# Kernel optimization log

Hardware: AMD Instinct MI355X
Metric: run time of the kernel (lower is better)

The kernel has to match this reference:

```python
import jax, jax.numpy as jnp
import numpy as np

D_MODEL = 2048
DT_RANK = 64


def setup_inputs() -> dict:
    key = jax.random.key(0)
    ks = jax.random.split(key, 9)
    x = jax.random.normal(ks[0], (4, 2048, D_MODEL), dtype=jnp.float32)
    A = jax.random.normal(ks[1], (D_MODEL, D_MODEL), dtype=jnp.float32)
    B = jax.random.normal(ks[2], (D_MODEL, D_MODEL), dtype=jnp.float32)
    C = jax.random.normal(ks[3], (D_MODEL, D_MODEL), dtype=jnp.float32)
    Dp = jax.random.normal(ks[4], (1, D_MODEL), dtype=jnp.float32)
    # dt_project: Linear(d_model -> dt_rank); dt_project_out: Linear(dt_rank -> d_model)
    lim1 = 1.0 / np.sqrt(D_MODEL)
    W1 = jax.random.uniform(ks[5], (DT_RANK, D_MODEL), minval=-lim1, maxval=lim1, dtype=jnp.float32)
    b1 = jax.random.uniform(ks[6], (DT_RANK,), minval=-lim1, maxval=lim1, dtype=jnp.float32)
    lim2 = 1.0 / np.sqrt(DT_RANK)
    W2 = jax.random.uniform(ks[7], (D_MODEL, DT_RANK), minval=-lim2, maxval=lim2, dtype=jnp.float32)
    b2 = jax.random.uniform(ks[8], (D_MODEL,), minval=-lim2, maxval=lim2, dtype=jnp.float32)
    return {"x": x, "A": A, "B": B, "C": C, "Dp": Dp, "W1": W1, "b1": b1, "W2": W2, "b2": b2}


def reference(x, A, B, C, Dp, W1, b1, W2, b2):
    # dt = Linear_out(gelu(Linear_in(x)))  -- torch uses exact (erf) gelu
    h = jax.nn.gelu(jnp.einsum('bld,rd->blr', x, W1) + b1, approximate=False)
    dt = jnp.einsum('blr,dr->bld', h, W2) + b2
    # per-timestep loop collapses to one batched GEMM: x @ (A+B+C)
    out = jnp.einsum('bld,ds->bls', x, A + B + C)
    return out * dt + Dp  # Dp broadcasts (1, d_model)
```

## Files before the change

kernel.cpp:

```cpp
#include <hip/hip_runtime.h>
#include <stdint.h>

#define D 2048
#define R 64
#define M_TOTAL 8192

typedef float f32x4 __attribute__((ext_vector_type(4)));
typedef __bf16 bf16x8 __attribute__((ext_vector_type(8)));
typedef unsigned short u16x8 __attribute__((ext_vector_type(8)));
typedef unsigned short u16x4 __attribute__((ext_vector_type(4)));

__device__ __forceinline__ unsigned short f2bf(float f) {
  unsigned u = __builtin_bit_cast(unsigned, f);
  u += 0x7FFFu + ((u >> 16) & 1u);
  return (unsigned short)(u >> 16);
}

__device__ __forceinline__ void gload_lds16(const void* g, void* l) {
  __builtin_amdgcn_global_load_lds(
      (const __attribute__((address_space(1))) void*)g,
      (__attribute__((address_space(3))) void*)l, 16, 0, 0);
}

__global__ void prep_kernel(const float* __restrict__ x, const float* __restrict__ A,
                            const float* __restrict__ B, const float* __restrict__ C,
                            const float* __restrict__ w1, const float* __restrict__ w2,
                            unsigned short* __restrict__ xbf, unsigned short* __restrict__ st,
                            unsigned short* __restrict__ w1bf, unsigned short* __restrict__ w2bf) {
  __shared__ unsigned short lds[64][68];
  int t = threadIdx.x;
  if (blockIdx.x < 1024) {
    int tk = blockIdx.x >> 5, tn = blockIdx.x & 31;
    int k0 = tk * 64, n0 = tn * 64;
#pragma unroll
    for (int q = 0; q < 4; ++q) {
      int row = q * 16 + (t >> 4);
      int col = (t & 15) * 4;
      size_t off = (size_t)(k0 + row) * D + n0 + col;
      float4 a = *(const float4*)(A + off);
      float4 b = *(const float4*)(B + off);
      float4 c = *(const float4*)(C + off);
      u16x4 o = { f2bf(a.x + b.x + c.x), f2bf(a.y + b.y + c.y),
                  f2bf(a.z + b.z + c.z), f2bf(a.w + b.w + c.w) };
      *(u16x4*)(&lds[row][col]) = o;
    }
    __syncthreads();
    int n = t >> 2, kc = (t & 3) * 16;
    u16x8 v0, v1;
#pragma unroll
    for (int jj = 0; jj < 8; ++jj) v0[jj] = lds[kc + jj][n];
#pragma unroll
    for (int jj = 0; jj < 8; ++jj) v1[jj] = lds[kc + 8 + jj][n];
    size_t ooff = (size_t)(n0 + n) * D + k0 + kc;
    *(u16x8*)(st + ooff) = v0;
    *(u16x8*)(st + ooff + 8) = v1;
  } else {
    const int NX4 = (M_TOTAL * D) / 4;
    const int NW4 = (R * D) / 4;
    int stride = 1024 * 256;
    for (int i = (blockIdx.x - 1024) * 256 + t; i < NX4 + 2 * NW4; i += stride) {
      const float4* src; unsigned short* dst; int j;
      if (i < NX4)            { src = (const float4*)x;  dst = xbf;  j = i; }
      else if (i < NX4 + NW4) { src = (const float4*)w1; dst = w1bf; j = i - NX4; }
      else                    { src = (const float4*)w2; dst = w2bf; j = i - NX4 - NW4; }
      float4 v = src[j];
      u16x4 o = { f2bf(v.x), f2bf(v.y), f2bf(v.z), f2bf(v.w) };
      *(u16x4*)(dst + (size_t)j * 4) = o;
    }
  }
}

__global__ __launch_bounds__(256) void h_kernel(const unsigned short* __restrict__ xbf,
                                                const unsigned short* __restrict__ w1bf,
                                                const float* __restrict__ b1,
                                                unsigned short* __restrict__ hbf) {
  __shared__ unsigned short sX[4 * 2048];
  __shared__ unsigned short sW[4 * 2048];
  int t = threadIdx.x;
  int w = t >> 6, l = t & 63;
  int lm = l & 15, lk = l >> 4;
  int m0 = blockIdx.x * 64;
  f32x4 acc[4] = {};

  const unsigned short* srcX = xbf + (size_t)(m0 + (t & 63)) * D + (t >> 6) * 8;
  const unsigned short* srcW = w1bf + (size_t)(t & 63) * D + (t >> 6) * 8;
  const int dstw = w * 512;

#define HSTAGE(kt) do { \
    gload_lds16(srcX + (kt) * 32, sX + ((kt) & 3) * 2048 + dstw); \
    gload_lds16(srcW + (kt) * 32, sW + ((kt) & 3) * 2048 + dstw); } while (0)

  HSTAGE(0); HSTAGE(1); HSTAGE(2);
  asm volatile("s_waitcnt vmcnt(4)" ::: "memory");
  __builtin_amdgcn_s_barrier();

#pragma unroll 1
  for (int kt = 0; kt < 64; ++kt) {
    const unsigned short* bX = sX + (kt & 3) * 2048;
    const unsigned short* bW = sW + (kt & 3) * 2048;
    bf16x8 a = __builtin_bit_cast(bf16x8, *(const u16x8*)(bX + lk * 512 + (w * 16 + lm) * 8));
    bf16x8 bw[4];
#pragma unroll
    for (int j = 0; j < 4; ++j)
      bw[j] = __builtin_bit_cast(bf16x8, *(const u16x8*)(bW + lk * 512 + (j * 16 + lm) * 8));
    if (kt + 3 < 64) HSTAGE(kt + 3);
#pragma unroll
    for (int j = 0; j < 4; ++j)
      acc[j] = __builtin_amdgcn_mfma_f32_16x16x32_bf16(a, bw[j], acc[j], 0, 0, 0);
    if (kt < 61) asm volatile("s_waitcnt vmcnt(4)" ::: "memory");
    else         asm volatile("s_waitcnt vmcnt(0)" ::: "memory");
    __builtin_amdgcn_s_barrier();
  }
#undef HSTAGE

  int m_base = m0 + w * 16 + lk * 4;
#pragma unroll
  for (int j = 0; j < 4; ++j) {
    int n = j * 16 + lm;
    float bv = b1[n];
#pragma unroll
    for (int r = 0; r < 4; ++r) {
      float v = acc[j][r] + bv;
      float g = 0.5f * v * (1.0f + erff(v * 0.70710678118654752f));
      hbf[(size_t)(m_base + r) * R + n] = f2bf(g);
    }
  }
}

__global__ __launch_bounds__(512, 2) void gemm_kernel(
    const unsigned short* __restrict__ xbf, const unsigned short* __restrict__ st,
    const unsigned short* __restrict__ hbf, const unsigned short* __restrict__ w2bf,
    const float* __restrict__ b2, const float* __restrict__ dp,
    float* __restrict__ out) {
  __shared__ unsigned short sA[2 * 16384];
  __shared__ unsigned short sB[2 * 16384];
  const int tid = threadIdx.x;
  const int w = tid >> 6, l = tid & 63, lk = l >> 4, lm = l & 15;
  const int wm = w >> 2, wn = w & 3;
  int bid = blockIdx.x;
  int wg = (bid & 7) * 32 + (bid >> 3);
  int mb = wg >> 3, nb = wg & 7;
  int m0 = mb * 256, n0 = nb * 256;

  const int kg = (tid & 7) ^ ((tid >> 3) & 7);
  const unsigned short* gA = xbf + (size_t)(m0 + (tid >> 3)) * D + kg * 8;
  const unsigned short* gB = st + (size_t)(n0 + (tid >> 3)) * D + kg * 8;
  const int dstw = w * 512;

  const int s7 = lm & 7;
  const int gsw0 = (lk ^ s7) * 8;
  const int gsw1 = ((4 | lk) ^ s7) * 8;
  const int arow = (wm * 128 + lm) * 64;
  const int brow = (wn * 64 + lm) * 64;

  f32x4 acc[8][4] = {};

#define STAGE(gptr, sbuf, T, h) do { \
    const unsigned short* g_ = (gptr) + (size_t)((h) * 128) * D + (T) * 64; \
    unsigned short* d_ = (sbuf) + (((T) & 1) * 16384 + (h) * 8192 + dstw); \
    gload_lds16(g_, d_); \
    gload_lds16(g_ + 64 * D, d_ + 4096); } while (0)

#define LD8(buf, off) __builtin_bit_cast(bf16x8, *(const u16x8*)((buf) + (off)))

  STAGE(gA, sA, 0, 0); STAGE(gA, sA, 0, 1);
  STAGE(gB, sB, 0, 0); STAGE(gB, sB, 0, 1);
  STAGE(gB, sB, 1, 0); STAGE(gB, sB, 1, 1);
  asm volatile("s_waitcnt vmcnt(4)" ::: "memory");
  __builtin_amdgcn_s_barrier();

  const int NT = D / 64;
#pragma unroll 1
  for (int kt = 0; kt < NT; ++kt) {
    const unsigned short* bufA = sA + (kt & 1) * 16384;
    const unsigned short* bufB = sB + (kt & 1) * 16384;
    bf16x8 a[4][2], b0[2][2], b1[2][2];

    #pragma unroll
    for (int i = 0; i < 4; ++i) {
      a[i][0] = LD8(bufA, arow + i * 1024 + gsw0);
      a[i][1] = LD8(bufA, arow + i * 1024 + gsw1);
    }
    #pragma unroll
    for (int j = 0; j < 2; ++j) {
      b0[j][0] = LD8(bufB, brow + j * 1024 + gsw0);
      b0[j][1] = LD8(bufB, brow + j * 1024 + gsw1);
    }
    if (kt + 1 < NT) STAGE(gA, sA, kt + 1, 0);
    __builtin_amdgcn_s_barrier();
    asm volatile("s_waitcnt lgkmcnt(0)" ::: "memory");
    __builtin_amdgcn_s_setprio(1);
    #pragma unroll
    for (int i = 0; i < 4; ++i)
      #pragma unroll
      for (int j = 0; j < 2; ++j) {
        acc[i][j] = __builtin_amdgcn_mfma_f32_16x16x32_bf16(a[i][0], b0[j][0], acc[i][j], 0, 0, 0);
        acc[i][j] = __builtin_amdgcn_mfma_f32_16x16x32_bf16(a[i][1], b0[j][1], acc[i][j], 0, 0, 0);
      }
    __builtin_amdgcn_s_setprio(0);
    __builtin_amdgcn_s_barrier();

    #pragma unroll
    for (int j = 0; j < 2; ++j) {
      b1[j][0] = LD8(bufB, brow + (j + 2) * 1024 + gsw0);
      b1[j][1] = LD8(bufB, brow + (j + 2) * 1024 + gsw1);
    }
    if (kt + 1 < NT) STAGE(gA, sA, kt + 1, 1);
    __builtin_amdgcn_s_barrier();
    asm volatile("s_waitcnt lgkmcnt(0)" ::: "memory");
    __builtin_amdgcn_s_setprio(1);
    #pragma unroll
    for (int i = 0; i < 4; ++i)
      #pragma unroll
      for (int j = 0; j < 2; ++j) {
        acc[i][j + 2] = __builtin_amdgcn_mfma_f32_16x16x32_bf16(a[i][0], b1[j][0], acc[i][j + 2], 0, 0, 0);
        acc[i][j + 2] = __builtin_amdgcn_mfma_f32_16x16x32_bf16(a[i][1], b1[j][1], acc[i][j + 2], 0, 0, 0);
      }
    __builtin_amdgcn_s_setprio(0);
    __builtin_amdgcn_s_barrier();

    #pragma unroll
    for (int i = 0; i < 4; ++i) {
      a[i][0] = LD8(bufA, arow + (i + 4) * 1024 + gsw0);
      a[i][1] = LD8(bufA, arow + (i + 4) * 1024 + gsw1);
    }
    if (kt + 2 < NT) STAGE(gB, sB, kt + 2, 0);
    __builtin_amdgcn_s_barrier();
    asm volatile("s_waitcnt lgkmcnt(0)" ::: "memory");
    __builtin_amdgcn_s_setprio(1);
    #pragma unroll
    for (int i = 0; i < 4; ++i)
      #pragma unroll
      for (int j = 0; j < 2; ++j) {
        acc[i + 4][j + 2] = __builtin_amdgcn_mfma_f32_16x16x32_bf16(a[i][0], b1[j][0], acc[i + 4][j + 2], 0, 0, 0);
        acc[i + 4][j + 2] = __builtin_amdgcn_mfma_f32_16x16x32_bf16(a[i][1], b1[j][1], acc[i + 4][j + 2], 0, 0, 0);
      }
    __builtin_amdgcn_s_setprio(0);
    __builtin_amdgcn_s_barrier();

    if (kt + 2 < NT) STAGE(gB, sB, kt + 2, 1);
    __builtin_amdgcn_s_setprio(1);
    #pragma unroll
    for (int i = 0; i < 4; ++i)
      #pragma unroll
      for (int j = 0; j < 2; ++j) {
        acc[i + 4][j] = __builtin_amdgcn_mfma_f32_16x16x32_bf16(a[i][0], b0[j][0], acc[i + 4][j], 0, 0, 0);
        acc[i + 4][j] = __builtin_amdgcn_mfma_f32_16x16x32_bf16(a[i][1], b0[j][1], acc[i + 4][j], 0, 0, 0);
      }
    __builtin_amdgcn_s_setprio(0);
    if (kt < NT - 2) asm volatile("s_waitcnt vmcnt(4)" ::: "memory");
    else             asm volatile("s_waitcnt vmcnt(0)" ::: "memory");
    __builtin_amdgcn_s_barrier();
  }

  bf16x8 wb0[4], wb1[4];
  float b2v[4], dpv[4];
#pragma unroll
  for (int j = 0; j < 4; ++j) {
    int n = n0 + wn * 64 + j * 16 + lm;
    const u16x8* wp = (const u16x8*)(w2bf + (size_t)n * R + lk * 8);
    wb0[j] = __builtin_bit_cast(bf16x8, wp[0]);
    wb1[j] = __builtin_bit_cast(bf16x8, wp[4]);
    b2v[j] = b2[n];
    dpv[j] = dp[n];
  }
#pragma unroll
  for (int mi = 0; mi < 8; ++mi) {
    int hrow = m0 + wm * 128 + mi * 16 + lm;
    const u16x8* hp = (const u16x8*)(hbf + (size_t)hrow * R + lk * 8);
    bf16x8 ha0 = __builtin_bit_cast(bf16x8, hp[0]);
    bf16x8 ha1 = __builtin_bit_cast(bf16x8, hp[4]);
    int mbase = m0 + wm * 128 + mi * 16 + lk * 4;
#pragma unroll
    for (int j = 0; j < 4; ++j) {
      f32x4 dt = {};
      dt = __builtin_amdgcn_mfma_f32_16x16x32_bf16(ha0, wb0[j], dt, 0, 0, 0);
      dt = __builtin_amdgcn_mfma_f32_16x16x32_bf16(ha1, wb1[j], dt, 0, 0, 0);
      int n = n0 + wn * 64 + j * 16 + lm;
#pragma unroll
      for (int r = 0; r < 4; ++r) {
        float val = acc[mi][j][r] * (dt[r] + b2v[j]) + dpv[j];
        out[(size_t)(mbase + r) * D + n] = val;
      }
    }
  }
#undef STAGE
#undef LD8
}

extern "C" void kernel_launch(void* const* d_in, const int* in_sizes, int n_in,
                              void* d_out, int out_size, void* d_ws, size_t ws_size,
                              hipStream_t stream) {
  const float* x  = (const float*)d_in[0];
  const float* A  = (const float*)d_in[1];
  const float* B  = (const float*)d_in[2];
  const float* C  = (const float*)d_in[3];
  const float* Dp = (const float*)d_in[4];
  const float* W1 = (const float*)d_in[5];
  const float* b1 = (const float*)d_in[6];
  const float* W2 = (const float*)d_in[7];
  const float* b2 = (const float*)d_in[8];
  float* out = (float*)d_out;

  uint8_t* ws = (uint8_t*)d_ws;
  unsigned short* xbf  = (unsigned short*)ws;
  unsigned short* st   = (unsigned short*)(ws + (32u << 20));
  unsigned short* w1bf = (unsigned short*)(ws + (40u << 20));
  unsigned short* w2bf = (unsigned short*)(ws + (40u << 20) + (256u << 10));
  unsigned short* hbf  = (unsigned short*)(ws + (41u << 20));

  prep_kernel<<<2048, 256, 0, stream>>>(x, A, B, C, W1, W2, xbf, st, w1bf, w2bf);
  h_kernel<<<128, 256, 0, stream>>>(xbf, w1bf, b1, hbf);
  gemm_kernel<<<256, 512, 0, stream>>>(xbf, st, hbf, w2bf, b2, Dp, out);
}
```

Measured before the change: 118.9 us.

## Fuse x conversion and dt-projection GEMM into prep kernel; reschedule GEMM prefetch

New measurement: 119.0 us. Within noise of the previous version (+0.1%).

```diff
diff --git a/kernel.cpp b/kernel.cpp
--- a/kernel.cpp
+++ b/kernel.cpp
@@ -22,15 +22,70 @@
       (__attribute__((address_space(3))) void*)l, 16, 0, 0);
 }
 
-__global__ void prep_kernel(const float* __restrict__ x, const float* __restrict__ A,
-                            const float* __restrict__ B, const float* __restrict__ C,
-                            const float* __restrict__ w1, const float* __restrict__ w2,
-                            unsigned short* __restrict__ xbf, unsigned short* __restrict__ st,
-                            unsigned short* __restrict__ w1bf, unsigned short* __restrict__ w2bf) {
-  __shared__ unsigned short lds[64][68];
+__global__ __launch_bounds__(256) void prep_kernel(
+    const float* __restrict__ x, const float* __restrict__ A,
+    const float* __restrict__ B, const float* __restrict__ C,
+    const float* __restrict__ w1, const float* __restrict__ b1,
+    const float* __restrict__ w2,
+    unsigned short* __restrict__ xbf, unsigned short* __restrict__ st,
+    unsigned short* __restrict__ w2bf, unsigned short* __restrict__ hbf) {
+  __shared__ unsigned short plds[10240];
   int t = threadIdx.x;
-  if (blockIdx.x < 1024) {
-    int tk = blockIdx.x >> 5, tn = blockIdx.x & 31;
+  int bx = blockIdx.x;
+  if (bx < 128) {
+    int m0 = bx * 64;
+    int row = t >> 2, c8 = (t & 3) * 8;
+    const float* xp = x + (size_t)(m0 + row) * D + c8;
+    const float* wp = w1 + (size_t)row * D + c8;
+    unsigned short* xop = xbf + (size_t)(m0 + row) * D + c8;
+    unsigned short* sX = plds;
+    unsigned short* sW = plds + 5120;
+    int w = t >> 6, lm = t & 15, lk = (t & 63) >> 4;
+    f32x4 acc[4] = {};
+    float4 rx0 = *(const float4*)(xp);
+    float4 rx1 = *(const float4*)(xp + 4);
+    float4 rw0 = *(const float4*)(wp);
+    float4 rw1 = *(const float4*)(wp + 4);
+#pragma unroll 1
+    for (int kt = 0; kt < 64; ++kt) {
+      int buf = (kt & 1) * 2560;
+      u16x8 ox = { f2bf(rx0.x), f2bf(rx0.y), f2bf(rx0.z), f2bf(rx0.w),
+                   f2bf(rx1.x), f2bf(rx1.y), f2bf(rx1.z), f2bf(rx1.w) };
+      u16x8 ow = { f2bf(rw0.x), f2bf(rw0.y), f2bf(rw0.z), f2bf(rw0.w),
+                   f2bf(rw1.x), f2bf(rw1.y), f2bf(rw1.z), f2bf(rw1.w) };
+      *(u16x8*)(sX + buf + row * 40 + c8) = ox;
+      *(u16x8*)(sW + buf + row * 40 + c8) = ow;
+      *(u16x8*)(xop + kt * 32) = ox;
+      __syncthreads();
+      if (kt < 63) {
+        rx0 = *(const float4*)(xp + (kt + 1) * 32);
+        rx1 = *(const float4*)(xp + (kt + 1) * 32 + 4);
+        rw0 = *(const float4*)(wp + (kt + 1) * 32);
+        rw1 = *(const float4*)(wp + (kt + 1) * 32 + 4);
+      }
+      bf16x8 a = __builtin_bit_cast(bf16x8, *(const u16x8*)(sX + buf + (w * 16 + lm) * 40 + lk * 8));
+#pragma unroll
+      for (int j = 0; j < 4; ++j) {
+        bf16x8 b = __builtin_bit_cast(bf16x8, *(const u16x8*)(sW + buf + (j * 16 + lm) * 40 + lk * 8));
+        acc[j] = __builtin_amdgcn_mfma_f32_16x16x32_bf16(a, b, acc[j], 0, 0, 0);
+      }
+    }
+    int m_base = m0 + w * 16 + lk * 4;
+#pragma unroll
+    for (int j = 0; j < 4; ++j) {
+      int n = j * 16 + lm;
+      float bv = b1[n];
+#pragma unroll
+      for (int r = 0; r < 4; ++r) {
+        float v = acc[j][r] + bv;
+        float g = 0.5f * v * (1.0f + erff(v * 0.70710678118654752f));
+        hbf[(size_t)(m_base + r) * R + n] = f2bf(g);
+      }
+    }
+  } else if (bx < 1152) {
+    unsigned short (*lds)[68] = (unsigned short(*)[68])plds;
+    int id = bx - 128;
+    int tk = id >> 5, tn = id & 31;
     int k0 = tk * 64, n0 = tn * 64;
 #pragma unroll
     for (int q = 0; q < 4; ++q) {
@@ -55,74 +110,11 @@
     *(u16x8*)(st + ooff) = v0;
     *(u16x8*)(st + ooff + 8) = v1;
   } else {
-    const int NX4 = (M_TOTAL * D) / 4;
-    const int NW4 = (R * D) / 4;
-    int stride = 1024 * 256;
-    for (int i = (blockIdx.x - 1024) * 256 + t; i < NX4 + 2 * NW4; i += stride) {
-      const float4* src; unsigned short* dst; int j;
-      if (i < NX4)            { src = (const float4*)x;  dst = xbf;  j = i; }
-      else if (i < NX4 + NW4) { src = (const float4*)w1; dst = w1bf; j = i - NX4; }
-      else                    { src = (const float4*)w2; dst = w2bf; j = i - NX4 - NW4; }
-      float4 v = src[j];
+    const int NW4 = (D * R) / 4;
+    for (int i = (bx - 1152) * 256 + t; i < NW4; i += 8 * 256) {
+      float4 v = ((const float4*)w2)[i];
       u16x4 o = { f2bf(v.x), f2bf(v.y), f2bf(v.z), f2bf(v.w) };
-      *(u16x4*)(dst + (size_t)j * 4) = o;
-    }
-  }
-}
-
-__global__ __launch_bounds__(256) void h_kernel(const unsigned short* __restrict__ xbf,
-                                                const unsigned short* __restrict__ w1bf,
-                                                const float* __restrict__ b1,
-                                                unsigned short* __restrict__ hbf) {
-  __shared__ unsigned short sX[4 * 2048];
-  __shared__ unsigned short sW[4 * 2048];
-  int t = threadIdx.x;
-  int w = t >> 6, l = t & 63;
-  int lm = l & 15, lk = l >> 4;
-  int m0 = blockIdx.x * 64;
-  f32x4 acc[4] = {};
-
-  const unsigned short* srcX = xbf + (size_t)(m0 + (t & 63)) * D + (t >> 6) * 8;
-  const unsigned short* srcW = w1bf + (size_t)(t & 63) * D + (t >> 6) * 8;
-  const int dstw = w * 512;
-
-#define HSTAGE(kt) do { \
-    gload_lds16(srcX + (kt) * 32, sX + ((kt) & 3) * 2048 + dstw); \
-    gload_lds16(srcW + (kt) * 32, sW + ((kt) & 3) * 2048 + dstw); } while (0)
-
-  HSTAGE(0); HSTAGE(1); HSTAGE(2);
-  asm volatile("s_waitcnt vmcnt(4)" ::: "memory");
-  __builtin_amdgcn_s_barrier();
-
-#pragma unroll 1
-  for (int kt = 0; kt < 64; ++kt) {
-    const unsigned short* bX = sX + (kt & 3) * 2048;
-    const unsigned short* bW = sW + (kt & 3) * 2048;
-    bf16x8 a = __builtin_bit_cast(bf16x8, *(const u16x8*)(bX + lk * 512 + (w * 16 + lm) * 8));
-    bf16x8 bw[4];
-#pragma unroll
-    for (int j = 0; j < 4; ++j)
-      bw[j] = __builtin_bit_cast(bf16x8, *(const u16x8*)(bW + lk * 512 + (j * 16 + lm) * 8));
-    if (kt + 3 < 64) HSTAGE(kt + 3);
-#pragma unroll
-    for (int j = 0; j < 4; ++j)
-      acc[j] = __builtin_amdgcn_mfma_f32_16x16x32_bf16(a, bw[j], acc[j], 0, 0, 0);
-    if (kt < 61) asm volatile("s_waitcnt vmcnt(4)" ::: "memory");
-    else         asm volatile("s_waitcnt vmcnt(0)" ::: "memory");
-    __builtin_amdgcn_s_barrier();
-  }
-#undef HSTAGE
-
-  int m_base = m0 + w * 16 + lk * 4;
-#pragma unroll
-  for (int j = 0; j < 4; ++j) {
-    int n = j * 16 + lm;
-    float bv = b1[n];
-#pragma unroll
-    for (int r = 0; r < 4; ++r) {
-      float v = acc[j][r] + bv;
-      float g = 0.5f * v * (1.0f + erff(v * 0.70710678118654752f));
-      hbf[(size_t)(m_base + r) * R + n] = f2bf(g);
+      *(u16x4*)(w2bf + (size_t)i * 4) = o;
     }
   }
 }
@@ -165,8 +157,7 @@
 
   STAGE(gA, sA, 0, 0); STAGE(gA, sA, 0, 1);
   STAGE(gB, sB, 0, 0); STAGE(gB, sB, 0, 1);
-  STAGE(gB, sB, 1, 0); STAGE(gB, sB, 1, 1);
-  asm volatile("s_waitcnt vmcnt(4)" ::: "memory");
+  asm volatile("s_waitcnt vmcnt(0)" ::: "memory");
   __builtin_amdgcn_s_barrier();
 
   const int NT = D / 64;
@@ -186,7 +177,7 @@
       b0[j][0] = LD8(bufB, brow + j * 1024 + gsw0);
       b0[j][1] = LD8(bufB, brow + j * 1024 + gsw1);
     }
-    if (kt + 1 < NT) STAGE(gA, sA, kt + 1, 0);
+    if (kt + 1 < NT) { STAGE(gA, sA, kt + 1, 0); STAGE(gA, sA, kt + 1, 1); }
     __builtin_amdgcn_s_barrier();
     asm volatile("s_waitcnt lgkmcnt(0)" ::: "memory");
     __builtin_amdgcn_s_setprio(1);
@@ -205,7 +196,7 @@
       b1[j][0] = LD8(bufB, brow + (j + 2) * 1024 + gsw0);
       b1[j][1] = LD8(bufB, brow + (j + 2) * 1024 + gsw1);
     }
-    if (kt + 1 < NT) STAGE(gA, sA, kt + 1, 1);
+    if (kt + 1 < NT) STAGE(gB, sB, kt + 1, 0);
     __builtin_amdgcn_s_barrier();
     asm volatile("s_waitcnt lgkmcnt(0)" ::: "memory");
     __builtin_amdgcn_s_setprio(1);
@@ -224,7 +215,7 @@
       a[i][0] = LD8(bufA, arow + (i + 4) * 1024 + gsw0);
       a[i][1] = LD8(bufA, arow + (i + 4) * 1024 + gsw1);
     }
-    if (kt + 2 < NT) STAGE(gB, sB, kt + 2, 0);
+    if (kt + 1 < NT) STAGE(gB, sB, kt + 1, 1);
     __builtin_amdgcn_s_barrier();
     asm volatile("s_waitcnt lgkmcnt(0)" ::: "memory");
     __builtin_amdgcn_s_setprio(1);
@@ -238,7 +229,6 @@
     __builtin_amdgcn_s_setprio(0);
     __builtin_amdgcn_s_barrier();
 
-    if (kt + 2 < NT) STAGE(gB, sB, kt + 2, 1);
     __builtin_amdgcn_s_setprio(1);
     #pragma unroll
     for (int i = 0; i < 4; ++i)
@@ -248,8 +238,7 @@
         acc[i + 4][j] = __builtin_amdgcn_mfma_f32_16x16x32_bf16(a[i][1], b0[j][1], acc[i + 4][j], 0, 0, 0);
       }
     __builtin_amdgcn_s_setprio(0);
-    if (kt < NT - 2) asm volatile("s_waitcnt vmcnt(4)" ::: "memory");
-    else             asm volatile("s_waitcnt vmcnt(0)" ::: "memory");
+    asm volatile("s_waitcnt vmcnt(0)" ::: "memory");
     __builtin_amdgcn_s_barrier();
   }
 
@@ -305,11 +294,9 @@
   uint8_t* ws = (uint8_t*)d_ws;
   unsigned short* xbf  = (unsigned short*)ws;
   unsigned short* st   = (unsigned short*)(ws + (32u << 20));
-  unsigned short* w1bf = (unsigned short*)(ws + (40u << 20));
-  unsigned short* w2bf = (unsigned short*)(ws + (40u << 20) + (256u << 10));
+  unsigned short* w2bf = (unsigned short*)(ws + (40u << 20));
   unsigned short* hbf  = (unsigned short*)(ws + (41u << 20));
 
-  prep_kernel<<<2048, 256, 0, stream>>>(x, A, B, C, W1, W2, xbf, st, w1bf, w2bf);
-  h_kernel<<<128, 256, 0, stream>>>(xbf, w1bf, b1, hbf);
+  prep_kernel<<<1160, 256, 0, stream>>>(x, A, B, C, W1, b1, W2, xbf, st, w2bf, hbf);
   gemm_kernel<<<256, 512, 0, stream>>>(xbf, st, hbf, w2bf, b2, Dp, out);
 }
```
